# Performance work log

Hardware: AMD Instinct MI355X
Metric: run time of the kernel (lower is better)

Reference implementation:

```python
import jax, jax.numpy as jnp
import numpy as np

EMBED_DIM = 256
NUM_HEADS = 8
HEAD_DIM = EMBED_DIM // NUM_HEADS
SCALE = float(np.sqrt(HEAD_DIM))


def setup_inputs() -> dict:
    key = jax.random.key(0)
    ks = jax.random.split(key, 9)
    B, C, H, W = 4, EMBED_DIM, 48, 48
    s = 1.0 / np.sqrt(C)
    x = jax.random.normal(ks[0], (B, C, H, W), dtype=jnp.float32)
    # 1x1 convs == per-pixel channel matmuls; store as [out_c, in_c] weights + bias
    wq = jax.random.normal(ks[1], (C, C), dtype=jnp.float32) * s
    wk = jax.random.normal(ks[2], (C, C), dtype=jnp.float32) * s
    wv = jax.random.normal(ks[3], (C, C), dtype=jnp.float32) * s
    wo = jax.random.normal(ks[4], (C, C), dtype=jnp.float32) * s
    bq = jax.random.normal(ks[5], (C,), dtype=jnp.float32) * s
    bk = jax.random.normal(ks[6], (C,), dtype=jnp.float32) * s
    bv = jax.random.normal(ks[7], (C,), dtype=jnp.float32) * s
    bo = jax.random.normal(ks[8], (C,), dtype=jnp.float32) * s
    return {"x": x, "wq": wq, "bq": bq, "wk": wk, "bk": bk,
            "wv": wv, "bv": bv, "wo": wo, "bo": bo}


def reference(x, wq, bq, wk, bk, wv, bv, wo, bo):
    B, C, H, W = x.shape
    L = H * W
    xf = x.reshape(B, C, L)  # [B, C, L]
    def proj(w, b):
        y = jnp.einsum('oc,bcl->bol', w, xf) + b[None, :, None]
        return y.reshape(B, NUM_HEADS, HEAD_DIM, L)
    q = proj(wq, bq)  # [B, h, d, L]
    k = proj(wk, bk)
    v = proj(wv, bv)
    # scores: [B, h, Lq, Lk]
    attn = jnp.einsum('bhdq,bhdk->bhqk', q, k) / SCALE
    attn = jax.nn.softmax(attn, axis=-1)
    # dropout is identity in eval mode
    out = jnp.einsum('bhdk,bhqk->bhdq', v, attn)  # [B, h, d, L]
    out = out.reshape(B, C, L)
    out = jnp.einsum('oc,bcl->bol', wo, out) + bo[None, :, None]
    return out.reshape(B, C, H, W)
```

## Files before the change

kernel.cpp:

```cpp
#include <hip/hip_runtime.h>
#include <hip/hip_bf16.h>

typedef __attribute__((ext_vector_type(8))) short bf16x8;
typedef __attribute__((ext_vector_type(4))) float f32x4;

#define DEV static __device__ __forceinline__

constexpr int Cc = 256;
constexpr int Ll = 2304;
constexpr float SM_C = 0.25503486f;

#if __has_builtin(__builtin_amdgcn_exp2f)
#define EXP2(x) __builtin_amdgcn_exp2f(x)
#else
#define EXP2(x) exp2f(x)
#endif
#if __has_builtin(__builtin_amdgcn_rcpf)
#define RCP(x) __builtin_amdgcn_rcpf(x)
#else
#define RCP(x) (1.0f / (x))
#endif

DEV unsigned short f2bf(float f) {
  union { float f; unsigned u; } v; v.f = f;
  unsigned r = v.u + 0x7FFFu + ((v.u >> 16) & 1u);
  return (unsigned short)(r >> 16);
}

DEV unsigned short f2bfc(float f) {
  union { __hip_bfloat16 h; unsigned short u; } c;
  c.h = __float2bfloat16(f);
  return c.u;
}

__global__ __launch_bounds__(256) void k_xpose(const float* __restrict__ x,
                                               unsigned short* __restrict__ xt) {
  int b = blockIdx.z;
  int c0 = blockIdx.y * 32;
  int l = blockIdx.x * 256 + threadIdx.x;
  const float* xp = x + (size_t)b * Cc * Ll + l;
  unsigned short* op = xt + ((size_t)b * Ll + l) * Cc + c0;
  float v[32];
#pragma unroll
  for (int j = 0; j < 32; ++j) v[j] = xp[(size_t)(c0 + j) * Ll];
  unsigned u[16];
#pragma unroll
  for (int j = 0; j < 16; ++j)
    u[j] = (unsigned)f2bf(v[2 * j]) | ((unsigned)f2bf(v[2 * j + 1]) << 16);
  uint4* o4 = (uint4*)op;
#pragma unroll
  for (int j = 0; j < 4; ++j)
    o4[j] = make_uint4(u[4 * j], u[4 * j + 1], u[4 * j + 2], u[4 * j + 3]);
}

DEV void gemm_core(const float* __restrict__ W, const unsigned short* __restrict__ Bsrc,
                   unsigned short (*As)[264], unsigned short (*Bs)[264], f32x4 acc[4]) {
  int tid = threadIdx.x;
  const float4* wp = (const float4*)W;
#pragma unroll
  for (int j = 0; j < 16; ++j) {
    int idx = j * 256 + tid;
    int row = idx >> 6;
    int col = (idx & 63) * 4;
    float4 f = wp[idx];
    unsigned lo = (unsigned)f2bf(f.x) | ((unsigned)f2bf(f.y) << 16);
    unsigned hi = (unsigned)f2bf(f.z) | ((unsigned)f2bf(f.w) << 16);
    *(uint2*)&As[row][col] = make_uint2(lo, hi);
  }
  const uint4* bp = (const uint4*)Bsrc;
#pragma unroll
  for (int j = 0; j < 8; ++j) {
    int idx = j * 256 + tid;
    int row = idx >> 5;
    int col = (idx & 31) * 8;
    *(uint4*)&Bs[row][col] = bp[idx];
  }
  __syncthreads();
  int wave = tid >> 6, lane = tid & 63;
  int lm = wave * 16 + (lane & 15);
  int lk = (lane >> 4) * 8;
#pragma unroll
  for (int ks = 0; ks < 8; ++ks) {
    bf16x8 a = *(const bf16x8*)&As[lm][ks * 32 + lk];
#pragma unroll
    for (int nf = 0; nf < 4; ++nf) {
      bf16x8 bb = *(const bf16x8*)&Bs[nf * 16 + (lane & 15)][ks * 32 + lk];
      acc[nf] = __builtin_amdgcn_mfma_f32_16x16x32_bf16(a, bb, acc[nf], 0, 0, 0);
    }
  }
}

__global__ __launch_bounds__(256) void k_qkv(
    const unsigned short* __restrict__ xt,
    const float* __restrict__ wq, const float* __restrict__ bq,
    const float* __restrict__ wk, const float* __restrict__ bk,
    const float* __restrict__ wv, const float* __restrict__ bv,
    unsigned short* __restrict__ qt, unsigned short* __restrict__ kt,
    unsigned short* __restrict__ vm) {
  __shared__ __align__(16) unsigned short As[64][264];
  __shared__ __align__(16) unsigned short Bs[64][264];
  int z = blockIdx.z, b = z / 3, p = z % 3;
  const float* W = (p == 0) ? wq : (p == 1) ? wk : wv;
  const float* bias = (p == 0) ? bq : (p == 1) ? bk : bv;
  int m0 = blockIdx.y * 64, n0 = blockIdx.x * 64;
  f32x4 acc[4] = {};
  gemm_core(W + (size_t)m0 * 256, xt + ((size_t)b * Ll + n0) * 256, As, Bs, acc);
  int lane = threadIdx.x & 63, wave = threadIdx.x >> 6;
  int g = lane >> 4, cl = lane & 15;
  int ob = m0 + wave * 16 + g * 4;
  float b0 = bias[ob], b1 = bias[ob + 1], b2 = bias[ob + 2], b3 = bias[ob + 3];
  int h = ob >> 5, d0 = ob & 31;
  float sc = (p == 0) ? SM_C : 1.0f;
#pragma unroll
  for (int nf = 0; nf < 4; ++nf) {
    int l = n0 + nf * 16 + cl;
    float v0 = acc[nf][0] + b0, v1 = acc[nf][1] + b1;
    float v2 = acc[nf][2] + b2, v3 = acc[nf][3] + b3;
    if (p < 2) {
      v0 *= sc; v1 *= sc; v2 *= sc; v3 *= sc;
      unsigned short* dst = ((p == 0) ? qt : kt) +
          ((size_t)(b * 8 + h) * Ll + l) * 32 + d0;
      unsigned lo = (unsigned)f2bf(v0) | ((unsigned)f2bf(v1) << 16);
      unsigned hi = (unsigned)f2bf(v2) | ((unsigned)f2bf(v3) << 16);
      *(uint2*)dst = make_uint2(lo, hi);
    } else {
      size_t base = (size_t)(b * 8 + h) * 32 + d0;
      vm[(base + 0) * Ll + l] = f2bf(v0);
      vm[(base + 1) * Ll + l] = f2bf(v1);
      vm[(base + 2) * Ll + l] = f2bf(v2);
      vm[(base + 3) * Ll + l] = f2bf(v3);
    }
  }
}

__global__ __launch_bounds__(256) void k_attn(
    const unsigned short* __restrict__ qt,
    const unsigned short* __restrict__ kt,
    const unsigned short* __restrict__ vm,
    unsigned short* __restrict__ aot) {
  __shared__ __align__(16) unsigned short Ks[2][64][40];
  __shared__ __align__(16) unsigned short Vs[2][32][88];
  __shared__ __align__(16) unsigned short Ps[4][16][88];
  int bh = blockIdx.y, b = bh >> 3, h = bh & 7;
  int q0 = blockIdx.x * 64;
  int tid = threadIdx.x, wave = tid >> 6, lane = tid & 63;
  int g = lane >> 4, cl = lane & 15;

  const unsigned short* qb = qt + (size_t)bh * Ll * 32;
  const unsigned short* kb = kt + (size_t)bh * Ll * 32;
  const unsigned short* vb = vm + (size_t)bh * 32 * Ll;

  bf16x8 qf = *(const bf16x8*)&qb[(size_t)(q0 + wave * 16 + cl) * 32 + g * 8];

  bf16x8 ones;
#pragma unroll
  for (int i = 0; i < 8; ++i) ones[i] = (short)0x3F80;

  f32x4 oacc[2] = {};
  f32x4 osum = {};

  int krow = tid >> 2, kcol = (tid & 3) * 8;
  int vrow = tid >> 3, vcol = (tid & 7) * 8;

  {
    uint4 kr = *(const uint4*)&kb[(size_t)krow * 32 + kcol];
    uint4 vr = *(const uint4*)&vb[(size_t)vrow * Ll + vcol];
    *(uint4*)&Ks[0][krow][kcol] = kr;
    *(uint4*)&Vs[0][vrow][vcol] = vr;
  }

  constexpr int NT = Ll / 64;
  uint4 kr, vr;
  for (int t = 0; t < NT; ++t) {
    int cur = t & 1;
    if (t + 1 < NT) {
      int t0 = (t + 1) * 64;
      kr = *(const uint4*)&kb[(size_t)(t0 + krow) * 32 + kcol];
      vr = *(const uint4*)&vb[(size_t)vrow * Ll + t0 + vcol];
    }
    __syncthreads();

    f32x4 s[4];
#pragma unroll
    for (int f = 0; f < 4; ++f) {
      bf16x8 kf = *(const bf16x8*)&Ks[cur][f * 16 + cl][g * 8];
      f32x4 z = {};
      s[f] = __builtin_amdgcn_mfma_f32_16x16x32_bf16(qf, kf, z, 0, 0, 0);
    }
#pragma unroll
    for (int f = 0; f < 4; ++f)
#pragma unroll
      for (int r = 0; r < 4; ++r)
        Ps[wave][g * 4 + r][f * 16 + cl] = f2bfc(EXP2(s[f][r]));

#pragma unroll
    for (int ks = 0; ks < 2; ++ks) {
      bf16x8 pf = *(const bf16x8*)&Ps[wave][cl][ks * 32 + g * 8];
      osum = __builtin_amdgcn_mfma_f32_16x16x32_bf16(pf, ones, osum, 0, 0, 0);
#pragma unroll
      for (int nf = 0; nf < 2; ++nf) {
        bf16x8 vf = *(const bf16x8*)&Vs[cur][nf * 16 + cl][ks * 32 + g * 8];
        oacc[nf] = __builtin_amdgcn_mfma_f32_16x16x32_bf16(pf, vf, oacc[nf], 0, 0, 0);
      }
    }
    if (t + 1 < NT) {
      *(uint4*)&Ks[cur ^ 1][krow][kcol] = kr;
      *(uint4*)&Vs[cur ^ 1][vrow][vcol] = vr;
    }
  }

  int qrow = q0 + wave * 16 + g * 4;
#pragma unroll
  for (int r = 0; r < 4; ++r) {
    float inv = RCP(osum[r]);
#pragma unroll
    for (int nf = 0; nf < 2; ++nf) {
      aot[((size_t)b * Ll + qrow + r) * 256 + h * 32 + nf * 16 + cl] =
          f2bfc(oacc[nf][r] * inv);
    }
  }
}

__global__ __launch_bounds__(256) void k_oproj(
    const unsigned short* __restrict__ aot,
    const float* __restrict__ wo, const float* __restrict__ bo,
    float* __restrict__ out) {
  __shared__ __align__(16) unsigned short As[64][264];
  __shared__ __align__(16) unsigned short Bs[64][264];
  int b = blockIdx.z;
  int m0 = blockIdx.y * 64, n0 = blockIdx.x * 64;
  f32x4 acc[4] = {};
  gemm_core(wo + (size_t)m0 * 256, aot + ((size_t)b * Ll + n0) * 256, As, Bs, acc);
  int lane = threadIdx.x & 63, wave = threadIdx.x >> 6;
  int g = lane >> 4, cl = lane & 15;
  int ob = m0 + wave * 16 + g * 4;
  float b0 = bo[ob], b1 = bo[ob + 1], b2 = bo[ob + 2], b3 = bo[ob + 3];
#pragma unroll
  for (int nf = 0; nf < 4; ++nf) {
    int l = n0 + nf * 16 + cl;
    float* dst = out + ((size_t)b * 256 + ob) * Ll + l;
    dst[(size_t)0 * Ll] = acc[nf][0] + b0;
    dst[(size_t)1 * Ll] = acc[nf][1] + b1;
    dst[(size_t)2 * Ll] = acc[nf][2] + b2;
    dst[(size_t)3 * Ll] = acc[nf][3] + b3;
  }
}

extern "C" void kernel_launch(void* const* d_in, const int* in_sizes, int n_in,
                              void* d_out, int out_size, void* d_ws, size_t ws_size,
                              hipStream_t stream) {
  (void)in_sizes; (void)n_in; (void)out_size; (void)ws_size;
  const float* x  = (const float*)d_in[0];
  const float* wq = (const float*)d_in[1];
  const float* bq = (const float*)d_in[2];
  const float* wk = (const float*)d_in[3];
  const float* bk = (const float*)d_in[4];
  const float* wv = (const float*)d_in[5];
  const float* bv = (const float*)d_in[6];
  const float* wo = (const float*)d_in[7];
  const float* bo = (const float*)d_in[8];
  float* out = (float*)d_out;

  const size_t CH = (size_t)4 * Ll * Cc;
  unsigned short* xt = (unsigned short*)d_ws;
  unsigned short* qt = xt + CH;
  unsigned short* kt = xt + 2 * CH;
  unsigned short* vm = xt + 3 * CH;
  unsigned short* aot = xt;

  k_xpose<<<dim3(9, 8, 4), 256, 0, stream>>>(x, xt);
  k_qkv<<<dim3(36, 4, 12), 256, 0, stream>>>(xt, wq, bq, wk, bk, wv, bv, qt, kt, vm);
  k_attn<<<dim3(36, 32), 256, 0, stream>>>(qt, kt, vm, aot);
  k_oproj<<<dim3(36, 4, 4), 256, 0, stream>>>(aot, wo, bo, out);
}
```

Before: 165.3 us.

## Restructure attention with 32x32 MFMA, register P, and key-split waves; pre-convert weights

The attention kernel now uses 32x32x16 MFMAs. Each pair of waves splits the key tiles between them, and P is kept in registers and exchanged across lane halves with shuffles instead of going through shared memory. The two partial outputs and row sums are combined through shared memory at the end. Weights are converted to bf16 (with the softmax scale folded into Wq) once by a new kernel, so the GEMMs load A fragments straight from global memory instead of converting per block into LDS. This trades extra registers and a final reduction for fewer LDS round trips and a lower MFMA instruction count.

```diff
diff --git a/kernel.cpp b/kernel.cpp
--- a/kernel.cpp
+++ b/kernel.cpp
@@ -3,6 +3,7 @@
 
 typedef __attribute__((ext_vector_type(8))) short bf16x8;
 typedef __attribute__((ext_vector_type(4))) float f32x4;
+typedef __attribute__((ext_vector_type(16))) float f32x16;
 
 #define DEV static __device__ __forceinline__
 
@@ -33,6 +34,28 @@
   return c.u;
 }
 
+DEV unsigned packbf(float lo, float hi) {
+  return (unsigned)f2bfc(lo) | ((unsigned)f2bfc(hi) << 16);
+}
+
+__global__ __launch_bounds__(256) void k_wconv(
+    const float* __restrict__ wq, const float* __restrict__ wk,
+    const float* __restrict__ wv, const float* __restrict__ wo,
+    unsigned short* __restrict__ wb) {
+  int m = blockIdx.y;
+  const float* src = (m == 0) ? wq : (m == 1) ? wk : (m == 2) ? wv : wo;
+  float sc = (m == 0) ? SM_C : 1.0f;
+  int i = (blockIdx.x * 256 + threadIdx.x) * 8;
+  float4 f0 = *(const float4*)&src[i];
+  float4 f1 = *(const float4*)&src[i + 4];
+  uint4 o;
+  o.x = (unsigned)f2bf(f0.x * sc) | ((unsigned)f2bf(f0.y * sc) << 16);
+  o.y = (unsigned)f2bf(f0.z * sc) | ((unsigned)f2bf(f0.w * sc) << 16);
+  o.z = (unsigned)f2bf(f1.x * sc) | ((unsigned)f2bf(f1.y * sc) << 16);
+  o.w = (unsigned)f2bf(f1.z * sc) | ((unsigned)f2bf(f1.w * sc) << 16);
+  *(uint4*)&wb[(size_t)m * 65536 + i] = o;
+}
+
 __global__ __launch_bounds__(256) void k_xpose(const float* __restrict__ x,
                                                unsigned short* __restrict__ xt) {
   int b = blockIdx.z;
@@ -53,82 +76,67 @@
     o4[j] = make_uint4(u[4 * j], u[4 * j + 1], u[4 * j + 2], u[4 * j + 3]);
 }
 
-DEV void gemm_core(const float* __restrict__ W, const unsigned short* __restrict__ Bsrc,
-                   unsigned short (*As)[264], unsigned short (*Bs)[264], f32x4 acc[4]) {
+DEV void gemm_core2(const unsigned short* __restrict__ Wrow,
+                    const unsigned short* __restrict__ Bsrc,
+                    unsigned short (*Bs)[264], f32x4 acc[4]) {
   int tid = threadIdx.x;
-  const float4* wp = (const float4*)W;
-#pragma unroll
-  for (int j = 0; j < 16; ++j) {
-    int idx = j * 256 + tid;
-    int row = idx >> 6;
-    int col = (idx & 63) * 4;
-    float4 f = wp[idx];
-    unsigned lo = (unsigned)f2bf(f.x) | ((unsigned)f2bf(f.y) << 16);
-    unsigned hi = (unsigned)f2bf(f.z) | ((unsigned)f2bf(f.w) << 16);
-    *(uint2*)&As[row][col] = make_uint2(lo, hi);
-  }
+  int lane = tid & 63, cl = lane & 15, G = lane >> 4;
+  bf16x8 af[8];
+#pragma unroll
+  for (int ks = 0; ks < 8; ++ks) af[ks] = *(const bf16x8*)&Wrow[ks * 32];
   const uint4* bp = (const uint4*)Bsrc;
 #pragma unroll
   for (int j = 0; j < 8; ++j) {
     int idx = j * 256 + tid;
-    int row = idx >> 5;
-    int col = (idx & 31) * 8;
-    *(uint4*)&Bs[row][col] = bp[idx];
+    *(uint4*)&Bs[idx >> 5][(idx & 31) * 8] = bp[idx];
   }
   __syncthreads();
-  int wave = tid >> 6, lane = tid & 63;
-  int lm = wave * 16 + (lane & 15);
-  int lk = (lane >> 4) * 8;
 #pragma unroll
   for (int ks = 0; ks < 8; ++ks) {
-    bf16x8 a = *(const bf16x8*)&As[lm][ks * 32 + lk];
 #pragma unroll
     for (int nf = 0; nf < 4; ++nf) {
-      bf16x8 bb = *(const bf16x8*)&Bs[nf * 16 + (lane & 15)][ks * 32 + lk];
-      acc[nf] = __builtin_amdgcn_mfma_f32_16x16x32_bf16(a, bb, acc[nf], 0, 0, 0);
+      bf16x8 bb = *(const bf16x8*)&Bs[nf * 16 + cl][ks * 32 + G * 8];
+      acc[nf] = __builtin_amdgcn_mfma_f32_16x16x32_bf16(af[ks], bb, acc[nf], 0, 0, 0);
     }
   }
 }
 
 __global__ __launch_bounds__(256) void k_qkv(
-    const unsigned short* __restrict__ xt,
-    const float* __restrict__ wq, const float* __restrict__ bq,
-    const float* __restrict__ wk, const float* __restrict__ bk,
-    const float* __restrict__ wv, const float* __restrict__ bv,
+    const unsigned short* __restrict__ xt, const unsigned short* __restrict__ wb,
+    const float* __restrict__ bq, const float* __restrict__ bk,
+    const float* __restrict__ bv,
     unsigned short* __restrict__ qt, unsigned short* __restrict__ kt,
     unsigned short* __restrict__ vm) {
-  __shared__ __align__(16) unsigned short As[64][264];
   __shared__ __align__(16) unsigned short Bs[64][264];
   int z = blockIdx.z, b = z / 3, p = z % 3;
-  const float* W = (p == 0) ? wq : (p == 1) ? wk : wv;
   const float* bias = (p == 0) ? bq : (p == 1) ? bk : bv;
   int m0 = blockIdx.y * 64, n0 = blockIdx.x * 64;
-  f32x4 acc[4] = {};
-  gemm_core(W + (size_t)m0 * 256, xt + ((size_t)b * Ll + n0) * 256, As, Bs, acc);
   int lane = threadIdx.x & 63, wave = threadIdx.x >> 6;
   int g = lane >> 4, cl = lane & 15;
+  const unsigned short* Wrow =
+      wb + (size_t)p * 65536 + (size_t)(m0 + wave * 16 + cl) * 256 + g * 8;
+  f32x4 acc[4] = {};
+  gemm_core2(Wrow, xt + ((size_t)b * Ll + n0) * 256, Bs, acc);
   int ob = m0 + wave * 16 + g * 4;
-  float b0 = bias[ob], b1 = bias[ob + 1], b2 = bias[ob + 2], b3 = bias[ob + 3];
+  float sc = (p == 0) ? SM_C : 1.0f;
+  float b0 = bias[ob] * sc, b1 = bias[ob + 1] * sc;
+  float b2 = bias[ob + 2] * sc, b3 = bias[ob + 3] * sc;
   int h = ob >> 5, d0 = ob & 31;
-  float sc = (p == 0) ? SM_C : 1.0f;
 #pragma unroll
   for (int nf = 0; nf < 4; ++nf) {
     int l = n0 + nf * 16 + cl;
     float v0 = acc[nf][0] + b0, v1 = acc[nf][1] + b1;
     float v2 = acc[nf][2] + b2, v3 = acc[nf][3] + b3;
     if (p < 2) {
-      v0 *= sc; v1 *= sc; v2 *= sc; v3 *= sc;
       unsigned short* dst = ((p == 0) ? qt : kt) +
           ((size_t)(b * 8 + h) * Ll + l) * 32 + d0;
-      unsigned lo = (unsigned)f2bf(v0) | ((unsigned)f2bf(v1) << 16);
-      unsigned hi = (unsigned)f2bf(v2) | ((unsigned)f2bf(v3) << 16);
-      *(uint2*)dst = make_uint2(lo, hi);
+      *(uint2*)dst = make_uint2(packbf(v0, v1), packbf(v2, v3));
     } else {
       size_t base = (size_t)(b * 8 + h) * 32 + d0;
-      vm[(base + 0) * Ll + l] = f2bf(v0);
-      vm[(base + 1) * Ll + l] = f2bf(v1);
-      vm[(base + 2) * Ll + l] = f2bf(v2);
-      vm[(base + 3) * Ll + l] = f2bf(v3);
+      vm[(base + 0) * Ll + l] = f2bfc(v0);
+      vm[(base + 1) * Ll + l] = f2bfc(v1);
+      vm[(base + 2) * Ll + l] = f2bfc(v2);
+      vm[(base + 3) * Ll + l] = f2bfc(v3);
     }
   }
 }
@@ -139,100 +147,135 @@
     const unsigned short* __restrict__ vm,
     unsigned short* __restrict__ aot) {
   __shared__ __align__(16) unsigned short Ks[2][64][40];
-  __shared__ __align__(16) unsigned short Vs[2][32][88];
-  __shared__ __align__(16) unsigned short Ps[4][16][88];
+  __shared__ __align__(16) unsigned short Vs[2][32][72];
+  __shared__ float Osh[2][32][33];
+  __shared__ float Ssh[2][32];
   int bh = blockIdx.y, b = bh >> 3, h = bh & 7;
   int q0 = blockIdx.x * 64;
   int tid = threadIdx.x, wave = tid >> 6, lane = tid & 63;
-  int g = lane >> 4, cl = lane & 15;
+  int qsub = wave >> 1, sstr = wave & 1;
+  int hi = lane >> 5, c = lane & 31;
 
   const unsigned short* qb = qt + (size_t)bh * Ll * 32;
   const unsigned short* kb = kt + (size_t)bh * Ll * 32;
   const unsigned short* vb = vm + (size_t)bh * 32 * Ll;
 
-  bf16x8 qf = *(const bf16x8*)&qb[(size_t)(q0 + wave * 16 + cl) * 32 + g * 8];
+  bf16x8 qf[2];
+  qf[0] = *(const bf16x8*)&qb[(size_t)(q0 + qsub * 32 + c) * 32 + hi * 8];
+  qf[1] = *(const bf16x8*)&qb[(size_t)(q0 + qsub * 32 + c) * 32 + 16 + hi * 8];
 
   bf16x8 ones;
 #pragma unroll
   for (int i = 0; i < 8; ++i) ones[i] = (short)0x3F80;
 
-  f32x4 oacc[2] = {};
-  f32x4 osum = {};
+  f32x16 oacc = {};
+  f32x16 osum = {};
 
   int krow = tid >> 2, kcol = (tid & 3) * 8;
   int vrow = tid >> 3, vcol = (tid & 7) * 8;
 
   {
-    uint4 kr = *(const uint4*)&kb[(size_t)krow * 32 + kcol];
-    uint4 vr = *(const uint4*)&vb[(size_t)vrow * Ll + vcol];
-    *(uint4*)&Ks[0][krow][kcol] = kr;
-    *(uint4*)&Vs[0][vrow][vcol] = vr;
-  }
-
-  constexpr int NT = Ll / 64;
-  uint4 kr, vr;
-  for (int t = 0; t < NT; ++t) {
-    int cur = t & 1;
-    if (t + 1 < NT) {
-      int t0 = (t + 1) * 64;
-      kr = *(const uint4*)&kb[(size_t)(t0 + krow) * 32 + kcol];
-      vr = *(const uint4*)&vb[(size_t)vrow * Ll + t0 + vcol];
-    }
+    uint4 k0 = *(const uint4*)&kb[(size_t)krow * 32 + kcol];
+    uint4 k1 = *(const uint4*)&kb[(size_t)(64 + krow) * 32 + kcol];
+    uint4 v0 = *(const uint4*)&vb[(size_t)vrow * Ll + vcol];
+    uint4 v1 = *(const uint4*)&vb[(size_t)vrow * Ll + 64 + vcol];
+    *(uint4*)&Ks[0][krow][kcol] = k0;
+    *(uint4*)&Ks[1][krow][kcol] = k1;
+    *(uint4*)&Vs[0][vrow][vcol] = v0;
+    *(uint4*)&Vs[1][vrow][vcol] = v1;
+  }
+
+  uint4 kr0, kr1, vr0, vr1;
+  for (int j = 0; j < 18; ++j) {
     __syncthreads();
-
-    f32x4 s[4];
-#pragma unroll
-    for (int f = 0; f < 4; ++f) {
-      bf16x8 kf = *(const bf16x8*)&Ks[cur][f * 16 + cl][g * 8];
-      f32x4 z = {};
-      s[f] = __builtin_amdgcn_mfma_f32_16x16x32_bf16(qf, kf, z, 0, 0, 0);
-    }
-#pragma unroll
-    for (int f = 0; f < 4; ++f)
-#pragma unroll
-      for (int r = 0; r < 4; ++r)
-        Ps[wave][g * 4 + r][f * 16 + cl] = f2bfc(EXP2(s[f][r]));
-
-#pragma unroll
-    for (int ks = 0; ks < 2; ++ks) {
-      bf16x8 pf = *(const bf16x8*)&Ps[wave][cl][ks * 32 + g * 8];
-      osum = __builtin_amdgcn_mfma_f32_16x16x32_bf16(pf, ones, osum, 0, 0, 0);
-#pragma unroll
-      for (int nf = 0; nf < 2; ++nf) {
-        bf16x8 vf = *(const bf16x8*)&Vs[cur][nf * 16 + cl][ks * 32 + g * 8];
-        oacc[nf] = __builtin_amdgcn_mfma_f32_16x16x32_bf16(pf, vf, oacc[nf], 0, 0, 0);
+    if (j < 17) {
+      int ta = (2 * j + 2) * 64, tb = ta + 64;
+      kr0 = *(const uint4*)&kb[(size_t)(ta + krow) * 32 + kcol];
+      kr1 = *(const uint4*)&kb[(size_t)(tb + krow) * 32 + kcol];
+      vr0 = *(const uint4*)&vb[(size_t)vrow * Ll + ta + vcol];
+      vr1 = *(const uint4*)&vb[(size_t)vrow * Ll + tb + vcol];
+    }
+    f32x16 p_[2];
+#pragma unroll
+    for (int fb = 0; fb < 2; ++fb) {
+      f32x16 z = {};
+#pragma unroll
+      for (int dh = 0; dh < 2; ++dh) {
+        bf16x8 kf = *(const bf16x8*)&Ks[sstr][fb * 32 + c][dh * 16 + hi * 8];
+        z = __builtin_amdgcn_mfma_f32_32x32x16_bf16(kf, qf[dh], z, 0, 0, 0);
       }
-    }
-    if (t + 1 < NT) {
-      *(uint4*)&Ks[cur ^ 1][krow][kcol] = kr;
-      *(uint4*)&Vs[cur ^ 1][vrow][vcol] = vr;
-    }
-  }
-
-  int qrow = q0 + wave * 16 + g * 4;
-#pragma unroll
-  for (int r = 0; r < 4; ++r) {
-    float inv = RCP(osum[r]);
-#pragma unroll
-    for (int nf = 0; nf < 2; ++nf) {
-      aot[((size_t)b * Ll + qrow + r) * 256 + h * 32 + nf * 16 + cl] =
-          f2bfc(oacc[nf][r] * inv);
+      p_[fb] = z;
+    }
+#pragma unroll
+    for (int fb = 0; fb < 2; ++fb)
+#pragma unroll
+      for (int r = 0; r < 16; ++r) p_[fb][r] = EXP2(p_[fb][r]);
+    unsigned Wd[8][2];
+#pragma unroll
+    for (int fb = 0; fb < 2; ++fb)
+#pragma unroll
+      for (int u = 0; u < 4; ++u) {
+        Wd[fb * 4 + u][0] = packbf(p_[fb][4 * u + 0], p_[fb][4 * u + 1]);
+        Wd[fb * 4 + u][1] = packbf(p_[fb][4 * u + 2], p_[fb][4 * u + 3]);
+      }
+#pragma unroll
+    for (int ks = 0; ks < 4; ++ks) {
+      int e0 = 2 * ks, e1 = 2 * ks + 1;
+      unsigned t0 = hi ? Wd[e0][0] : Wd[e1][0];
+      unsigned t1 = hi ? Wd[e0][1] : Wd[e1][1];
+      unsigned o0 = (unsigned)__shfl_xor((int)t0, 32);
+      unsigned o1 = (unsigned)__shfl_xor((int)t1, 32);
+      union { bf16x8 v; unsigned u[4]; } pa;
+      pa.u[0] = hi ? o0 : Wd[e0][0];
+      pa.u[1] = hi ? o1 : Wd[e0][1];
+      pa.u[2] = hi ? Wd[e1][0] : o0;
+      pa.u[3] = hi ? Wd[e1][1] : o1;
+      bf16x8 vf = *(const bf16x8*)&Vs[sstr][c][ks * 16 + hi * 8];
+      oacc = __builtin_amdgcn_mfma_f32_32x32x16_bf16(pa.v, vf, oacc, 0, 0, 0);
+      osum = __builtin_amdgcn_mfma_f32_32x32x16_bf16(pa.v, ones, osum, 0, 0, 0);
+    }
+    __syncthreads();
+    if (j < 17) {
+      *(uint4*)&Ks[0][krow][kcol] = kr0;
+      *(uint4*)&Ks[1][krow][kcol] = kr1;
+      *(uint4*)&Vs[0][vrow][vcol] = vr0;
+      *(uint4*)&Vs[1][vrow][vcol] = vr1;
+    }
+  }
+
+  if (sstr == 1) {
+#pragma unroll
+    for (int r = 0; r < 16; ++r) {
+      int qrl = (r & 3) + 8 * (r >> 2) + 4 * hi;
+      Osh[qsub][qrl][c] = oacc[r];
+      if (c == 0) Ssh[qsub][qrl] = osum[r];
+    }
+  }
+  __syncthreads();
+  if (sstr == 0) {
+#pragma unroll
+    for (int r = 0; r < 16; ++r) {
+      int qrl = (r & 3) + 8 * (r >> 2) + 4 * hi;
+      float ot = oacc[r] + Osh[qsub][qrl][c];
+      float st = osum[r] + Ssh[qsub][qrl];
+      float val = ot * RCP(st);
+      aot[((size_t)b * Ll + q0 + qsub * 32 + qrl) * 256 + h * 32 + c] = f2bfc(val);
     }
   }
 }
 
 __global__ __launch_bounds__(256) void k_oproj(
-    const unsigned short* __restrict__ aot,
-    const float* __restrict__ wo, const float* __restrict__ bo,
-    float* __restrict__ out) {
-  __shared__ __align__(16) unsigned short As[64][264];
+    const unsigned short* __restrict__ aot, const unsigned short* __restrict__ wb,
+    const float* __restrict__ bo, float* __restrict__ out) {
   __shared__ __align__(16) unsigned short Bs[64][264];
   int b = blockIdx.z;
   int m0 = blockIdx.y * 64, n0 = blockIdx.x * 64;
-  f32x4 acc[4] = {};
-  gemm_core(wo + (size_t)m0 * 256, aot + ((size_t)b * Ll + n0) * 256, As, Bs, acc);
   int lane = threadIdx.x & 63, wave = threadIdx.x >> 6;
   int g = lane >> 4, cl = lane & 15;
+  const unsigned short* Wrow =
+      wb + (size_t)3 * 65536 + (size_t)(m0 + wave * 16 + cl) * 256 + g * 8;
+  f32x4 acc[4] = {};
+  gemm_core2(Wrow, aot + ((size_t)b * Ll + n0) * 256, Bs, acc);
   int ob = m0 + wave * 16 + g * 4;
   float b0 = bo[ob], b1 = bo[ob + 1], b2 = bo[ob + 2], b3 = bo[ob + 3];
 #pragma unroll
@@ -266,10 +309,12 @@
   unsigned short* qt = xt + CH;
   unsigned short* kt = xt + 2 * CH;
   unsigned short* vm = xt + 3 * CH;
+  unsigned short* wbq = xt + 4 * CH;
   unsigned short* aot = xt;
 
+  k_wconv<<<dim3(32, 4), 256, 0, stream>>>(wq, wk, wv, wo, wbq);
   k_xpose<<<dim3(9, 8, 4), 256, 0, stream>>>(x, xt);
-  k_qkv<<<dim3(36, 4, 12), 256, 0, stream>>>(xt, wq, bq, wk, bk, wv, bv, qt, kt, vm);
+  k_qkv<<<dim3(36, 4, 12), 256, 0, stream>>>(xt, wbq, bq, bk, bv, qt, kt, vm);
   k_attn<<<dim3(36, 32), 256, 0, stream>>>(qt, kt, vm, aot);
-  k_oproj<<<dim3(36, 4, 4), 256, 0, stream>>>(aot, wo, bo, out);
-}
+  k_oproj<<<dim3(36, 4, 4), 256, 0, stream>>>(aot, wbq, bo, out);
+}
```

New measurement: 202.9 us. 22.7% more time.
